# Optimization experiments

Measured on AMD Instinct MI355X. Metric: run time of the kernel, lower is better.

## Reference

```python
import jax, jax.numpy as jnp
import numpy as np

DIMS = [1536, 2048, 2560, 3072, 1792, 2304, 2816, 2048, 2560, 3328]

def _ln(x, g, b, eps=1e-5):
    m = jnp.mean(x, -1, keepdims=True)
    v = jnp.mean((x - m) ** 2, -1, keepdims=True)
    return (x - m) / jnp.sqrt(v + eps) * g + b

def _gelu(x):
    return jax.nn.gelu(x, approximate=False)

def _mish(x):
    return x * jnp.tanh(jax.nn.softplus(x))

_ACTS = [jax.nn.silu, _gelu, _mish, jax.nn.relu, jax.nn.selu, jnp.tanh, jax.nn.softplus, jax.nn.elu]

def _renorm_sparse_topk(probs, active_k, max_k):
    vals, idx = jax.lax.top_k(probs, max_k)
    mask = (jnp.arange(max_k)[None, :] < active_k[:, None]).astype(probs.dtype)
    n = probs.shape[0]
    sparse = jnp.zeros_like(probs).at[jnp.arange(n)[:, None], idx].set(vals * mask)
    return sparse / jnp.clip(jnp.sum(sparse, -1, keepdims=True), 1e-6, None)

def setup_inputs():
    N, IN, OUT, E, M, S, SUB, DST, INNER, SH = 2048, 1024, 10, 10, 24, 4, 4, 40, 768, 2048
    DMAX = max(DIMS)
    ks = iter(jax.random.split(jax.random.key(0), 80))
    def p(shape, std=0.02):
        return jax.random.normal(next(ks), shape, jnp.float32) * std
    eu = np.zeros((E, DMAX, IN), np.float32)
    ed = np.zeros((E, OUT, DMAX), np.float32)
    for i in range(E):
        d = DIMS[i % len(DIMS)]
        eu[i, :d] = np.asarray(p((d, IN), 0.02))
        ed[i, :, :d] = np.asarray(p((OUT, d), 0.01))
    return {
        'x': jax.random.normal(next(ks), (N, IN), jnp.float32),
        'weight': p((OUT, IN), 0.03), 'bias': p((OUT,), 0.01),
        'shared_up_w': p((SH, IN)), 'shared_down_w': p((OUT, SH), 0.01),
        'shared_norm_g': jnp.ones((OUT,)), 'shared_norm_b': jnp.zeros((OUT,)),
        'shared_scale': jnp.asarray(1.0, jnp.float32),
        'memory_keys': p((M, IN)), 'memory_values_init': p((M, IN)),
        'memory_query_w': p((IN, IN), 0.01), 'memory_out_w': p((OUT, IN), 0.01),
        'mem_wgate_w': p((M, 2 * IN), 0.01), 'mem_wgate_b': jnp.zeros((M,)),
        'mem_wval_w': p((IN, IN), 0.01), 'mem_wval_b': jnp.zeros((IN,)),
        'depth_q_w': p((IN, IN), 0.01), 'depth_k_w': p((IN, IN), 0.01),
        'depth_v_w': p((IN, IN), 0.01), 'depth_out_w': p((OUT, IN), 0.01),
        'cell_ln_g': jnp.ones((S, IN)), 'cell_ln_b': jnp.zeros((S, IN)),
        'cell_fc1_w': p((S, INNER, IN)), 'cell_fc1_b': jnp.zeros((S, INNER)),
        'cell_fc2_w': p((S, IN, INNER)), 'cell_fc2_b': jnp.zeros((S, IN)),
        'ssm_a_w': p((DST, IN), 0.01), 'ssm_a_b': jnp.zeros((DST,)),
        'ssm_b_w': p((IN, DST), 0.01), 'ssm_b_b': jnp.zeros((IN,)),
        'mor_sub_w': p((SUB, E, IN)), 'mor_sub_b': jnp.zeros((SUB, E)),
        'mor_mix_w': p((SUB, IN)), 'mor_mix_b': jnp.zeros((SUB,)),
        'expert_bias': jnp.zeros((E,)),
        'budget_w': p((4, IN)), 'budget_b': jnp.zeros((4,)),
        'experts_up': jnp.asarray(eu), 'experts_down': jnp.asarray(ed),
        'expert_norm_g': jnp.ones((E, OUT)), 'expert_norm_b': jnp.zeros((E, OUT)),
        'halt_w': p((S, 1, IN), 0.01), 'halt_b': jnp.full((S, 1), -2.0, jnp.float32),
        'alpha': jnp.asarray(0.1, jnp.float32), 'beta': jnp.asarray(0.1, jnp.float32),
    }

def reference(x, weight, bias, shared_up_w, shared_down_w, shared_norm_g, shared_norm_b, shared_scale, memory_keys, memory_values_init, memory_query_w, memory_out_w, mem_wgate_w, mem_wgate_b, mem_wval_w, mem_wval_b, depth_q_w, depth_k_w, depth_v_w, depth_out_w, cell_ln_g, cell_ln_b, cell_fc1_w, cell_fc1_b, cell_fc2_w, cell_fc2_b, ssm_a_w, ssm_a_b, ssm_b_w, ssm_b_b, mor_sub_w, mor_sub_b, mor_mix_w, mor_mix_b, expert_bias, budget_w, budget_b, experts_up, experts_down, expert_norm_g, expert_norm_b, halt_w, halt_b, alpha, beta):
    in_dim = x.shape[-1]
    x_flat = x.reshape(-1, in_dim)
    n = x_flat.shape[0]
    base = x_flat @ weight.T + bias
    shared = _ln(jax.nn.silu(x_flat @ shared_up_w.T) @ shared_down_w.T, shared_norm_g, shared_norm_b)
    mem_vals = jnp.broadcast_to(memory_values_init[None], (n,) + memory_values_init.shape)
    current = x_flat
    total = jnp.zeros_like(base)
    cum_halt = jnp.zeros((n, 1), x.dtype)
    bank = []
    mem_scale = in_dim ** -0.5
    steps = cell_ln_g.shape[0]
    n_exp = expert_bias.shape[0]
    max_topk = min(4, n_exp)
    for step in range(steps):
        mq = current @ memory_query_w.T
        mem_attn = jax.nn.softmax((mq @ memory_keys.T) * mem_scale, -1)  # [n, M]
        mem_ctx = jnp.einsum('nm,nmd->nd', mem_attn, mem_vals)
        if bank:
            ds = jnp.stack(bank, 1)  # [n, s, d]
            q = current @ depth_q_w.T
            k = ds @ depth_k_w.T
            v = ds @ depth_v_w.T
            attn = jax.nn.softmax(jnp.einsum('nd,nsd->ns', q, k) * mem_scale, -1)
            depth_ctx = jnp.einsum('ns,nsd->nd', attn, v)
        else:
            depth_ctx = jnp.zeros_like(current)
        ssm_corr = jnp.tanh(current @ ssm_a_w.T + ssm_a_b) @ ssm_b_w.T + ssm_b_b
        enriched = current + 0.34 * mem_ctx + 0.22 * depth_ctx + 0.18 * ssm_corr
        h = _gelu(_ln(enriched, cell_ln_g[step], cell_ln_b[step]) @ cell_fc1_w[step].T + cell_fc1_b[step])
        current = enriched + h @ cell_fc2_w[step].T + cell_fc2_b[step]
        bank.append(current)
        sub = jnp.einsum('nd,sed->nse', current, mor_sub_w) + mor_sub_b[None]
        mix = jax.nn.softmax(current @ mor_mix_w.T + mor_mix_b, -1)
        gate_probs = jax.nn.softmax(jnp.einsum('ns,nse->ne', mix, sub) + expert_bias, -1)
        budget = 1 + jnp.argmax(jax.nn.softmax(current @ budget_w.T + budget_b, -1), -1)
        sg = _renorm_sparse_topk(gate_probs, budget, max_topk)
        expert_logits = jnp.zeros_like(base)
        for i in range(n_exp):
            d = DIMS[i % len(DIMS)]
            hh = _ACTS[i % len(_ACTS)](current @ experts_up[i, :d, :].T)
            eo = _ln(hh @ experts_down[i, :, :d].T, expert_norm_g[i], expert_norm_b[i])
            expert_logits = expert_logits + sg[:, i:i + 1] * eo
        step_logits = expert_logits + 0.22 * (mem_ctx @ memory_out_w.T) + 0.14 * (depth_ctx @ depth_out_w.T)
        surprise = 1.0 - jnp.max(sg, -1, keepdims=True)  # [n, 1]
        wg = jax.nn.softmax(jnp.concatenate([current, mem_ctx], -1) @ mem_wgate_w.T + mem_wgate_b, -1)
        wv = (current @ mem_wval_w.T + mem_wval_b)[:, None, :]
        mem_vals = mem_vals + surprise[..., None] * wg[..., None] * (wv - mem_vals)
        halt = jax.nn.sigmoid((current + 0.2 * mem_ctx + 0.1 * depth_ctx) @ halt_w[step].T + halt_b[step])
        remaining = 1.0 - cum_halt
        total = total + remaining * step_logits
        cum_halt = cum_halt + remaining * halt
    total = total / float(steps)
    out = base + shared_scale * shared + (alpha + 1e-4) * total + beta * (current @ memory_out_w.T)
    return out.reshape(x.shape[:-1] + (out.shape[-1],))
```

## Files before the change

### kernel.cpp

```cpp
#include <hip/hip_runtime.h>
#include <stdint.h>

#define N_TOK 2048
#define IN_D  1024
#define NEXP  10
#define NSTEP 4
#define INNER 768
#define SHD   2048
#define DMAX  3328
#define DSUM  24064

typedef __attribute__((ext_vector_type(4))) float f32x4;
typedef __attribute__((ext_vector_type(8))) short bf16x8;

__device__ const int c_dims[10] = {1536,2048,2560,3072,1792,2304,2816,2048,2560,3328};
__device__ const int c_offs[10] = {0,1536,3584,6144,9216,11008,13312,16128,18176,20736};
__device__ const int c_acts[10] = {0,1,2,3,4,5,6,7,0,1};
__device__ const int c_cum[11]  = {0,12,28,48,72,86,104,126,142,162,188};

__device__ __forceinline__ float wred(float v){
#pragma unroll
  for (int s = 32; s > 0; s >>= 1) v += __shfl_xor(v, s, 64);
  return v;
}
// ... 113 lines not shown
}

__global__ void build_routew(const float* __restrict__ msw, const float* __restrict__ mmw,
                             const float* __restrict__ bw, const float* __restrict__ wgw,
                             const float* __restrict__ hw, const float* __restrict__ mow,
                             const float* __restrict__ dow, uint16_t* __restrict__ Wh,
                             uint16_t* __restrict__ Wl){
  const int TOT = 4 * 128 * 3072;
  for (int i = blockIdx.x * 256 + threadIdx.x; i < TOT; i += gridDim.x * 256){
    int t = i / (128 * 3072);
    int rem = i - t * (128 * 3072);
    int row = rem / 3072, col = rem - row * 3072;
    float v = 0.f;
    if (row < 40){ if (col < 1024) v = msw[row * 1024 + col]; }
    else if (row < 44){ if (col < 1024) v = mmw[(row - 40) * 1024 + col]; }
    else if (row < 48){ if (col < 1024) v = bw[(row - 44) * 1024 + col]; }
    else if (row < 72){ if (col < 2048) v = wgw[(row - 48) * 2048 + col]; }
    else if (row == 72){
      if (col < 1024) v = hw[t * 1024 + col];
      else if (col < 2048) v = 0.2f * hw[t * 1024 + col - 1024];
      else v = 0.1f * hw[t * 1024 + col - 2048];
    }
    else if (row < 83){ if (col >= 1024 && col < 2048) v = mow[(row - 73) * 1024 + col - 1024]; }
    else if (row < 93){ if (col >= 2048) v = dow[(row - 83) * 1024 + col - 2048]; }
    else if (row < 103){ if (col < 1024) v = mow[(row - 93) * 1024 + col]; }
    uint16_t h = f2bf(v);
    Wh[i] = h; Wl[i] = f2bf(v - bf2f(h));
  }
}

enum { EPI_GELU=0, EPI_CUR=1, EPI_PRE=2, EPI_QROUTE=3 };

template<int EPI>
__global__ __launch_bounds__(256)
void gemm_sp(const uint16_t* __restrict__ Ah, const uint16_t* __restrict__ Al, int lda,
             const uint16_t* __restrict__ Wh, const uint16_t* __restrict__ Wl,
             const uint16_t* __restrict__ W2h, const uint16_t* __restrict__ W2l,
             const float* __restrict__ bias, const float* __restrict__ addend,
             float* __restrict__ D0, float* __restrict__ D1, float* __restrict__ D2,
             float* __restrict__ D3, uint8_t* __restrict__ o8,
             uint16_t* __restrict__ oH, uint16_t* __restrict__ oL,
             int K, int D)
{
  __shared__ __align__(16) uint16_t sm[4][2][4096];
  int tid = threadIdx.x, lane = tid & 63, wave = tid >> 6;
  int wr = wave >> 1, wc = wave & 1;
  int arow = lane & 15, agrp = lane >> 4;
  int rowBase = blockIdx.y * 128;
  bool isRoute = (EPI == EPI_QROUTE) && ((int)blockIdx.x < 4);
  const uint16_t* Wsh = isRoute ? W2h : Wh;
  const uint16_t* Wsl = isRoute ? W2l : Wl;
  int wst     = isRoute ? 3072 : K;
  int colBase = isRoute ? 0 : ((EPI == EPI_QROUTE ? (int)blockIdx.x - 4 : (int)blockIdx.x) * 128);
  int kBase   = isRoute ? (int)blockIdx.x * 768 : 0;
  int kLen    = isRoute ? 768 : K;
  f32x4 acc[4][4];
#pragma unroll
  for (int m = 0; m < 4; m++)
#pragma unroll
    for (int n = 0; n < 4; n++){ f32x4 z = {0.f,0.f,0.f,0.f}; acc[m][n] = z; }

#define STAGE_G(buf, k0) do { \
  _Pragma("unroll") \
  for (int s = 0; s < 2; s++){ \
    int u = tid + s * 256; \
    int rr = u >> 2; \
    int ch = (u & 3) ^ ((rr >> 1) & 3); \
    size_t ga = (size_t)(rowBase + rr) * lda + kBase + (k0) + ch * 8; \
    size_t gw = (size_t)(colBase + rr) * wst + kBase + (k0) + ch * 8; \
    gload16(&Ah[ga], &sm[0][buf][u << 3]); \
    gload16(&Al[ga], &sm[1][buf][u << 3]); \
    gload16(&Wsh[gw], &sm[2][buf][u << 3]); \
    gload16(&Wsl[gw], &sm[3][buf][u << 3]); \
  } } while(0)

  int nk = kLen >> 5;
  STAGE_G(0, 0);
  if (nk > 1) STAGE_G(1, 32);
  int perm = (arow >> 1) & 3;
#pragma unroll 1
  for (int ki = 0; ki < nk; ki++){
    int cb = ki & 1;
    if (ki + 1 < nk) asm volatile("s_waitcnt vmcnt(8)" ::: "memory");
    else             asm volatile("s_waitcnt vmcnt(0)" ::: "memory");
    __builtin_amdgcn_s_barrier();
    bf16x8 ah[4], al[4], bh[4], bl[4];
#pragma unroll
// ... 19 lines not shown
    __builtin_amdgcn_s_barrier();
    asm volatile("" ::: "memory");
    if (ki + 2 < nk) STAGE_G(cb, (ki + 2) << 5);
  }
#undef STAGE_G
#pragma unroll
  for (int m = 0; m < 4; m++){
#pragma unroll
    for (int n = 0; n < 4; n++){
      int col = colBase + wc*64 + n*16 + arow;
#pragma unroll
      for (int r2 = 0; r2 < 4; r2++){
        int row = rowBase + wr*64 + m*16 + agrp*4 + r2;
        float v = acc[m][n][r2];
        if (EPI == EPI_GELU){
          v += bias[col];
          v = 0.5f * v * (1.f + erff(v * 0.7071067811865475f));
          size_t idx = (size_t)row * D + col;
          uint16_t h = f2bf(v); oH[idx] = h; oL[idx] = f2bf(v - bf2f(h));
        }
        if (EPI == EPI_CUR){
          v += bias[col] + addend[(size_t)row * 1024 + col];
          D0[(size_t)row * 1024 + col] = v;
          size_t idx = (size_t)row * 3072 + col;
          uint16_t h = f2bf(v); oH[idx] = h; oL[idx] = f2bf(v - bf2f(h));
          o8[(size_t)row * 1024 + col] = f2fp8(v);
        }
        if (EPI == EPI_PRE){
          if (col < 2048) D0[(size_t)row * 2048 + col] = v / (1.f + expf(-v));
          else D1[(size_t)row * 128 + col - 2048] = v;
        }
        if (EPI == EPI_QROUTE){
          if (isRoute){
            D3[((size_t)blockIdx.x * N_TOK + row) * 128 + col] = v;
          } else {
            if (col < 1024) D0[(size_t)row * 1024 + col] = v;
            else if (col < 4096) D1[(size_t)row * 3072 + col - 1024] = v + bias[col - 1024];
            else if (col < 4160) D2[(size_t)row * 128 + col - 4096] = v;
          }
        }
      }
    }
  }
}

__global__ __launch_bounds__(256)
void expert_up_mfma(const uint8_t* __restrict__ A8, const uint8_t* __restrict__ U8,
                    const int* __restrict__ cnt, const int* __restrict__ gidx,
                    uint16_t* __restrict__ HH)
{
  int y = blockIdx.y;
  int e = 0;
#pragma unroll
  for (int i = 1; i < 11; i++) if (y >= c_cum[i]) e = i;
  int ct = y - c_cum[e];
  int dcols = c_dims[e];
  int ne = cnt[e];
  const uint8_t* W = U8 + (size_t)e * DMAX * IN_D + (size_t)ct * 128 * IN_D;

  __shared__ __align__(16) uint8_t smem[32768];
  int tid = threadIdx.x, lane = tid & 63, wave = tid >> 6;
  int wr = wave >> 1, wc = wave & 1;
  int arow = lane & 15, agrp = lane >> 4;
  int actid = c_acts[e];
  size_t base_e = (size_t)N_TOK * c_offs[e];
  int rHalf = tid >> 1;
  int half16 = (tid & 1) * 16;

#define STAGE_E(b, k0) do { \
    gload16b(&A8[(size_t)tok * IN_D + (k0) + half16], &smem[(b)*8192 + tid*16]); \
    gload16b(&W[(size_t)rHalf * IN_D + (k0) + half16], &smem[(b)*8192 + 4096 + tid*16]); \
  } while(0)

#pragma unroll 1
  for (int rowBase = blockIdx.x * 128; rowBase < ne; rowBase += 4 * 128){
    int slot = rowBase + rHalf;
    int tok = (slot < ne) ? gidx[e * N_TOK + slot] : 0;

    f32x4 acc[4][4];
#pragma unroll
    for (int m = 0; m < 4; m++)
#pragma unroll
      for (int n = 0; n < 4; n++){ f32x4 z = {0.f,0.f,0.f,0.f}; acc[m][n] = z; }

    STAGE_E(0, 0);
    STAGE_E(1, 32);
    STAGE_E(2, 64);
    int cb = 0;
#pragma unroll 1
    for (int ki = 0; ki < 32; ki++){
      if (ki < 30)       asm volatile("s_waitcnt vmcnt(4)" ::: "memory");
      else if (ki == 30) asm volatile("s_waitcnt vmcnt(2)" ::: "memory");
      else               asm volatile("s_waitcnt vmcnt(0)" ::: "memory");
      __builtin_amdgcn_s_barrier();
      long a[4], b[4];
#pragma unroll
      for (int m = 0; m < 4; m++)
        a[m] = *(const long*)&smem[cb*8192 + (wr*64 + m*16 + arow)*32 + agrp*8];
#pragma unroll
      for (int n = 0; n < 4; n++)
        b[n] = *(const long*)&smem[cb*8192 + 4096 + (wc*64 + n*16 + arow)*32 + agrp*8];
#pragma unroll
      for (int m = 0; m < 4; m++)
#pragma unroll
        for (int n = 0; n < 4; n++)
          acc[m][n] = __builtin_amdgcn_mfma_f32_16x16x32_fp8_fp8(a[m], b[n], acc[m][n], 0, 0, 0);
      __builtin_amdgcn_s_barrier();
      asm volatile("" ::: "memory");
      if (ki + 3 < 32) STAGE_E(cb, (ki + 3) << 5);
      cb = (cb == 2) ? 0 : cb + 1;
    }
    uint16_t* Ht = (uint16_t*)smem;
#pragma unroll
    for (int m = 0; m < 4; m++){
      int rb0 = wr*64 + m*16 + agrp*4;
#pragma unroll
      for (int n = 0; n < 4; n++){
        int col = wc*64 + n*16 + arow;
#pragma unroll
        for (int r2 = 0; r2 < 4; r2++){
          int row = rb0 + r2;
          float v = actf(actid, acc[m][n][r2]);
          Ht[row * 128 + (col ^ ((row & 7) << 3))] = f2bf(v);
        }
      }
    }
    __syncthreads();
#pragma unroll
    for (int i = 0; i < 8; i++){
      int c = tid + i * 256;
      int row = c >> 4, chunk = c & 15;
      int schunk = (chunk & 8) | ((chunk ^ row) & 7);
      int4 val = *(const int4*)&Ht[row * 128 + schunk * 8];
      *(int4*)&HH[base_e + (size_t)(rowBase + row) * dcols
                  + (size_t)ct * 128 + chunk * 8] = val;
    }
    __syncthreads();
  }
#undef STAGE_E
}

__global__ __launch_bounds__(256)
void ctx_enr_kernel(const float* __restrict__ qaux, const float* __restrict__ dqbuf,
                    const float* __restrict__ Ac, const float* __restrict__ W0,
                    const float* __restrict__ W1, const float* __restrict__ W2,
                    const float* __restrict__ mvi,
                    const float* __restrict__ t0, const float* __restrict__ t1,
                    const float* __restrict__ t2, const float* __restrict__ cur,
                    const float* __restrict__ sab, const float* __restrict__ sbw,
                    const float* __restrict__ sbb, const float* __restrict__ lng,
                    const float* __restrict__ lnbv,
                    float* __restrict__ enr, uint16_t* __restrict__ lnh,
                    uint16_t* __restrict__ lnl, uint16_t* __restrict__ Arh,
                    uint16_t* __restrict__ Arl, int t)
{
  int row = blockIdx.x, tid = threadIdx.x;
  __shared__ float su[24], ss[3], s40[40], red[12], redm[8];
  if (tid < 64){
    float pj = (tid < 24) ? qaux[(size_t)row * 128 + tid] * 0.03125f : -1e30f;
    float mx = wmax(pj);
    float ex = (tid < 24) ? expf(pj - mx) : 0.f;
    float sum = wred(ex);
    float attn = ex / sum;
    if (tid < 24) su[tid] = attn * Ac[row * 24 + tid];
    float w0v = (t > 0 && tid < 24) ? W0[row * 24 + tid] : 0.f;
    float s0 = wred(attn * w0v);
    float w1v = (t > 1 && tid < 24) ? W1[row * 24 + tid] : 0.f;
    float s1 = wred(attn * w1v);
    float w2v = (t > 2 && tid < 24) ? W2[row * 24 + tid] : 0.f;
    float s2 = wred(attn * w2v);
    if (tid == 0){ ss[0] = s0; ss[1] = s1; ss[2] = s2; }
    if (tid < 40) s40[tid] = tanhf(qaux[(size_t)row * 128 + 24 + tid] + sab[tid]);
  }
  size_t tb = (size_t)row * 3072;
  if (t > 0){
    float a0 = 0.f, a1 = 0.f, a2 = 0.f;
#pragma unroll
    for (int j = 0; j < 4; j++){
      int d = tid + j * 256;
      float dq = dqbuf[(size_t)row * 1024 + d];
      a0 = fmaf(dq, t0[tb + d], a0);
      if (t > 1) a1 = fmaf(dq, t1[tb + d], a1);
      if (t > 2) a2 = fmaf(dq, t2[tb + d], a2);
    }
    a0 = wred(a0); a1 = wred(a1); a2 = wred(a2);
    if ((tid & 63) == 0){ int w = tid >> 6; red[w] = a0; red[4+w] = a1; red[8+w] = a2; }
  }
  __syncthreads();
  float e0 = 0.f, e1 = 0.f, e2 = 0.f;
// ... 31 lines not shown
#pragma unroll
    for (int o = 0; o < 40; o++) sv = fmaf(s40[o], sbw[d * 40 + o], sv);
    float v = cur[idx] + 0.34f * mv + 0.22f * dv + 0.18f * sv;
    uint16_t mh = f2bf(mv);
    Arh[ar + 1024 + d] = mh; Arl[ar + 1024 + d] = f2bf(mv - bf2f(mh));
    uint16_t dh = f2bf(dv);
    Arh[ar + 2048 + d] = dh; Arl[ar + 2048 + d] = f2bf(dv - bf2f(dh));
    ev[j] = v; part += v;
  }
  part = wred(part);
  if ((tid & 63) == 0) redm[tid >> 6] = part;
  __syncthreads();
  float mean = (redm[0] + redm[1] + redm[2] + redm[3]) * (1.f / 1024.f);
  float vp = 0.f;
#pragma unroll
  for (int j = 0; j < 4; j++){ float dd = ev[j] - mean; vp += dd * dd; }
  vp = wred(vp);
  if ((tid & 63) == 0) redm[4 + (tid >> 6)] = vp;
  __syncthreads();
  float var = (redm[4] + redm[5] + redm[6] + redm[7]) * (1.f / 1024.f);
  float rs = 1.f / sqrtf(var + 1e-5f);
#pragma unroll
  for (int j = 0; j < 4; j++){
    int d = tid + j * 256;
    size_t idx = (size_t)row * IN_D + d;
    enr[idx] = ev[j];
    float v = (ev[j] - mean) * rs * lng[t * IN_D + d] + lnbv[t * IN_D + d];
    uint16_t h = f2bf(v);
    lnh[idx] = h;
    lnl[idx] = f2bf(v - bf2f(h));
  }
}

__global__ __launch_bounds__(256)
void route_fin(const float* __restrict__ ROq, const float* __restrict__ mmb,
               const float* __restrict__ msb, const float* __restrict__ ebias,
               const float* __restrict__ bb, const float* __restrict__ wgb,
               const float* __restrict__ hb,
               float* __restrict__ sg, float* __restrict__ haltb,
               float* __restrict__ Ac, float* __restrict__ W0,
               float* __restrict__ W1, float* __restrict__ W2,
               int* __restrict__ cnt, int* __restrict__ gidx,
               int* __restrict__ pos, float* __restrict__ routeS, int t)
{
  int row = blockIdx.x * 256 + threadIdx.x;
  int lane = threadIdx.x & 63;
  const size_t P = (size_t)N_TOK * 128;
  const float* r0 = ROq + (size_t)row * 128;
  const float* r1 = r0 + P;
  const float* r2 = r0 + 2 * P;
  const float* r3 = r0 + 3 * P;
  auto R = [&](int j){ return r0[j] + r1[j] + r2[j] + r3[j]; };
  float pm[4];
#pragma unroll
  for (int o = 0; o < 4; o++) pm[o] = R(40 + o) + mmb[o];
  float mmx = fmaxf(fmaxf(pm[0], pm[1]), fmaxf(pm[2], pm[3]));
  float msum = 0.f;
#pragma unroll
  for (int o = 0; o < 4; o++){ pm[o] = expf(pm[o] - mmx); msum += pm[o]; }
  float minv = 1.f / msum;
  float gl[10];
#pragma unroll
  for (int e = 0; e < 10; e++){
    float g = ebias[e];
#pragma unroll
    for (int s2 = 0; s2 < 4; s2++)
      g = fmaf(pm[s2] * minv, R(s2 * 10 + e) + msb[s2 * 10 + e], g);
    gl[e] = g;
  }
  float gmx = gl[0];
#pragma unroll
  for (int e = 1; e < 10; e++) gmx = fmaxf(gmx, gl[e]);
  float gs = 0.f;
#pragma unroll
  for (int e = 0; e < 10; e++){ gl[e] = expf(gl[e] - gmx); gs += gl[e]; }
  float ginv = 1.f / gs;
#pragma unroll
  for (int e = 0; e < 10; e++) gl[e] *= ginv;
  float pb0 = R(44) + bb[0], pb1 = R(45) + bb[1], pb2 = R(46) + bb[2], pb3 = R(47) + bb[3];
  int bud = 1; float bbest = pb0;
  if (pb1 > bbest){ bbest = pb1; bud = 2; }
  if (pb2 > bbest){ bbest = pb2; bud = 3; }
  if (pb3 > bbest){ bbest = pb3; bud = 4; }
  float tv[4]; int ti[4]; unsigned used = 0;
#pragma unroll
  for (int j = 0; j < 4; j++){
    float best = -1e30f; int bi = 0;
#pragma unroll
    for (int e = 0; e < 10; e++){
      bool ok = (!((used >> e) & 1u)) && (gl[e] > best);
      if (ok){ best = gl[e]; bi = e; }
    }
    tv[j] = best; ti[j] = bi; used |= (1u << bi);
  }
  float ssum = tv[0];
  if (bud > 1) ssum += tv[1];
  if (bud > 2) ssum += tv[2];
  if (bud > 3) ssum += tv[3];
  float den = fmaxf(ssum, 1e-6f);
  float sup = 1.f - tv[0] / den;
  float sgv[10];
#pragma unroll
  for (int e = 0; e < 10; e++){
    float sv = 0.f;
#pragma unroll
    for (int j = 0; j < 4; j++) if (j < bud && ti[j] == e) sv = tv[j] / den;
    sgv[e] = sv;
    sg[row * 10 + e] = sv;
  }
  float pw[24];
#pragma unroll
  for (int m = 0; m < 24; m++) pw[m] = R(48 + m) + wgb[m];
  float wmx2 = pw[0];
#pragma unroll
  for (int m = 1; m < 24; m++) wmx2 = fmaxf(wmx2, pw[m]);
  float wsum = 0.f;
#pragma unroll
  for (int m = 0; m < 24; m++){ pw[m] = expf(pw[m] - wmx2); wsum += pw[m]; }
  float winv = 1.f / wsum;
#pragma unroll
  for (int m = 0; m < 24; m++){
    float c = sup * pw[m] * winv;
    float om = 1.f - c;
    Ac[row * 24 + m] *= om;
    if (t > 0) W0[row * 24 + m] *= om;
    if (t > 1) W1[row * 24 + m] *= om;
    if (t > 2) W2[row * 24 + m] *= om;
    if (t == 0)      W0[row * 24 + m] = c;
    else if (t == 1) W1[row * 24 + m] = c;
    else if (t == 2) W2[row * 24 + m] = c;
  }
  haltb[row] = 1.f / (1.f + expf(-(R(72) + hb[t])));
#pragma unroll
  for (int i = 0; i < 30; i++) routeS[row * 32 + i] = R(73 + i);
#pragma unroll
  for (int e = 0; e < 10; e++){
    bool act = sgv[e] != 0.f;
    unsigned long long mask = __ballot(act);
    int cw = __popcll(mask);
    int b0 = 0;
    if (lane == 0 && cw > 0) b0 = atomicAdd(&cnt[e], cw);
    b0 = __shfl(b0, 0, 64);
    if (act){
      int slot = b0 + __popcll(mask & ((1ull << lane) - 1ull));
      gidx[e * N_TOK + slot] = row;
      pos[row * 10 + e] = slot;
    }
  }
}

__global__ __launch_bounds__(256)
void downfin_kernel(const uint16_t* __restrict__ HH, const int* __restrict__ pos,
                    const float* __restrict__ ED, const float* __restrict__ sg,
                    const float* __restrict__ eng, const float* __restrict__ enb,
                    const float* __restrict__ routeS, const float* __restrict__ haltb,
                    float* __restrict__ total, float* __restrict__ cumh)
{
  int lane = threadIdx.x & 63;
  int row = blockIdx.x * 4 + (threadIdx.x >> 6);
  float out[10] = {};
  for (int e = 0; e < NEXP; e++){
    float g = sg[row * 10 + e];
    if (g != 0.0f){
      int d = c_dims[e];
      int slot = pos[row * 10 + e];
      const uint16_t* hr = HH + (size_t)N_TOK * c_offs[e] + (size_t)slot * d;
      const float* wd = ED + (size_t)e * 10 * DMAX;
      float p[10] = {};
      for (int k = lane * 4; k < d; k += 256){
        uint2 hv = *(const uint2*)&hr[k];
        float h0 = bf2f((uint16_t)hv.x), h1 = bf2f((uint16_t)(hv.x >> 16));
        float h2 = bf2f((uint16_t)hv.y), h3 = bf2f((uint16_t)(hv.y >> 16));
#pragma unroll
        for (int o = 0; o < 10; o++){
          float4 w4 = *(const float4*)&wd[o * DMAX + k];
          p[o] = fmaf(h0, w4.x, fmaf(h1, w4.y, fmaf(h2, w4.z, fmaf(h3, w4.w, p[o]))));
        }
      }
#pragma unroll
      for (int o = 0; o < 10; o++) p[o] = wred(p[o]);
      float mean = 0.f;
#pragma unroll
      for (int o = 0; o < 10; o++) mean += p[o];
      mean *= 0.1f;
      float var = 0.f;
#pragma unroll
      for (int o = 0; o < 10; o++){ float dd = p[o] - mean; var += dd * dd; }
      var *= 0.1f;
      float rs = 1.f / sqrtf(var + 1e-5f);
#pragma unroll
      for (int o = 0; o < 10; o++)
        out[o] += g * ((p[o] - mean) * rs * eng[e * 10 + o] + enb[e * 10 + o]);
    }
  }
  if (lane == 0){
    const float* r = routeS + (size_t)row * 32;
    float rem = 1.f - cumh[row];
#pragma unroll
    for (int o = 0; o < 10; o++)
      total[row * 10 + o] += rem * (out[o] + 0.22f * r[o] + 0.14f * r[10 + o]);
    cumh[row] += rem * haltb[row];
  }
}

__global__ __launch_bounds__(256)
void shared_kernel(const float* __restrict__ shpre, const float* __restrict__ sdw,
                   const float* __restrict__ g, const float* __restrict__ b,
                   float* __restrict__ outp)
{
  int lane = threadIdx.x & 63;
  int row = blockIdx.x * 4 + (threadIdx.x >> 6);
  const float* xr = shpre + (size_t)row * SHD;
  float p[10];
#pragma unroll
  for (int o = 0; o < 10; o++) p[o] = 0.f;
  for (int k = lane; k < SHD; k += 64){
    float xv = xr[k];
#pragma unroll
    for (int o = 0; o < 10; o++) p[o] = fmaf(xv, sdw[o * SHD + k], p[o]);
  }
#pragma unroll
  for (int o = 0; o < 10; o++) p[o] = wred(p[o]);
  float mean = 0.f;
#pragma unroll
  for (int o = 0; o < 10; o++) mean += p[o];
  mean *= 0.1f;
  float var = 0.f;
#pragma unroll
  for (int o = 0; o < 10; o++){ float dd = p[o] - mean; var += dd * dd; }
  var *= 0.1f;
  float rs = 1.f / sqrtf(var + 1e-5f);
  if (lane == 0){
#pragma unroll
    for (int o = 0; o < 10; o++) outp[row * 10 + o] = (p[o] - mean) * rs * g[o] + b[o];
// ... 125 lines not shown
  hipMemsetAsync(cbias, 0, 3072 * 4, stream);
  hipMemcpyAsync(cbias + 2048, wvb, 1024 * 4, hipMemcpyDeviceToDevice, stream);
  hipMemcpyAsync(cur, x, NI * 4, hipMemcpyDeviceToDevice, stream);
  fill1_kernel<<<(N_TOK * 24 + 255) / 256, 256, 0, stream>>>(Ac, N_TOK * 24);
  cvt_fp8_kernel<<<2048, 256, 0, stream>>>(eup, upbf8, (size_t)NEXP * DMAX * IN_D);

  split_strided<<<1024, 256, 0, stream>>>(x, Arh, Arl, N_TOK, 1024, 3072);
  split_kernel<<<1024, 256, 0, stream>>>(suw, preWh, preWl, (size_t)SHD * 1024);
  split_kernel<<<256, 256, 0, stream>>>(saw, preWh + (size_t)2072*1024, preWl + (size_t)2072*1024, (size_t)40 * 1024);
  split_kernel<<<256, 256, 0, stream>>>(wgt, preWh + (size_t)2112*1024, preWl + (size_t)2112*1024, (size_t)10 * 1024);
  hipMemsetAsync(preWh + (size_t)2122*1024, 0, (size_t)54 * 1024 * 2, stream);
  hipMemsetAsync(preWl + (size_t)2122*1024, 0, (size_t)54 * 1024 * 2, stream);
  split_kernel<<<1024, 256, 0, stream>>>(dqw, qtWh, qtWl, W1M);
  split_kernel<<<1024, 256, 0, stream>>>(dkw, qtWh + W1M, qtWl + W1M, W1M);
  split_kernel<<<1024, 256, 0, stream>>>(dvw, qtWh + 2*W1M, qtWl + 2*W1M, W1M);
  split_kernel<<<1024, 256, 0, stream>>>(wvw, qtWh + 3*W1M, qtWl + 3*W1M, W1M);
  split_kernel<<<256, 256, 0, stream>>>(saw, qtWh + (size_t)4120*1024, qtWl + (size_t)4120*1024, (size_t)40 * 1024);
  hipMemsetAsync(qtWh + (size_t)4160*1024, 0, (size_t)64 * 1024 * 2, stream);
  hipMemsetAsync(qtWl + (size_t)4160*1024, 0, (size_t)64 * 1024 * 2, stream);
  k2_kernel<<<dim3(24, 4), 256, 0, stream>>>(keys, mqw, K2f);
  split_kernel<<<256, 256, 0, stream>>>(K2f, preWh + (size_t)2048*1024, preWl + (size_t)2048*1024, (size_t)24 * 1024);
  split_kernel<<<256, 256, 0, stream>>>(K2f, qtWh + (size_t)4096*1024, qtWl + (size_t)4096*1024, (size_t)24 * 1024);
  build_routew<<<2048, 256, 0, stream>>>(msw, mmw, bw, wgw, hw, mow, dow, rtWh, rtWl);
  split_kernel<<<1024, 256, 0, stream>>>(fc1w, fc1wh, fc1wl, WFC);
  split_kernel<<<1024, 256, 0, stream>>>(fc2w, fc2wh, fc2wl, WFC);

  gemm_sp<EPI_PRE><<<dim3(17, 16), 256, 0, stream>>>(
      Arh, Arl, 3072, preWh, preWl, nullptr, nullptr, nullptr, nullptr,
      shpre, qaux, nullptr, nullptr, nullptr, nullptr, nullptr, IN_D, 2176);
  shared_kernel<<<512, 256, 0, stream>>>(shpre, sdw, sng, snb, sharedp);

  float* trioB[3] = {trio0, trio1, trio2};

  for (int t = 0; t < NSTEP; t++){
    ctx_enr_kernel<<<2048, 256, 0, stream>>>(qaux, dqbuf, Ac, W0, W1, W2, mvi,
                                             trio0, trio1, trio2, cur, sab, sbw, sbb,
                                             clng, clnb, enr, lnh, lnl, Arh, Arl, t);
    gemm_sp<EPI_GELU><<<dim3(INNER/128, 16), 256, 0, stream>>>(
        lnh, lnl, 1024, fc1wh + (size_t)t * INNER * IN_D, fc1wl + (size_t)t * INNER * IN_D,
        nullptr, nullptr, fc1b + t * INNER, nullptr,
        nullptr, nullptr, nullptr, nullptr, nullptr, h7h, h7l, IN_D, INNER);
    gemm_sp<EPI_CUR><<<dim3(8, 16), 256, 0, stream>>>(
        h7h, h7l, 768, fc2wh + (size_t)t * IN_D * INNER, fc2wl + (size_t)t * IN_D * INNER,
        nullptr, nullptr, fc2b + t * IN_D, enr,
        cur, nullptr, nullptr, nullptr, A8, Arh, Arl, INNER, IN_D);
    gemm_sp<EPI_QROUTE><<<dim3(t < 3 ? 37 : 4, 16), 256, 0, stream>>>(
        Arh, Arl, 3072, qtWh, qtWl,
        rtWh + (size_t)t * 128 * 3072, rtWl + (size_t)t * 128 * 3072,
        cbias, nullptr, dqbuf, t < 3 ? trioB[t] : nullptr, qaux, routeQ,
        nullptr, nullptr, nullptr, IN_D, 4224);
    route_fin<<<8, 256, 0, stream>>>(routeQ, mmb, msb, ebias, bb, wgb, hb,
                                     sg, haltb, Ac, W0, W1, W2,
                                     cnt + t * 16, gidx, pos, routeS, t);
    expert_up_mfma<<<dim3(4, 188), 256, 0, stream>>>(A8, upbf8, cnt + t * 16, gidx, HHc);
    downfin_kernel<<<512, 256, 0, stream>>>(HHc, pos, edn, sg, eng, enb,
                                            routeS, haltb, total, cumh);
  }
  final_lite<<<8, 256, 0, stream>>>(qaux, bias, sharedp, total, routeS,
                                    sscale, alphap, betap, outp);
}
```

Before: 2.202 ms.

## Co-schedule independent kernels via horizontal fusion and swizzle expert LDS layout

The per-step ctx kernel for step t+1 now runs in the same launch as the expert-up GEMM of step t, and the expert-down/finalize work of step t-1 shares a launch with the fc1 GEMM of step t. Block-index ranges select which core runs, so fewer launches are needed and under-filled grids can overlap on the GPU. The expert-up kernel also swizzles its LDS staging and read offsets to cut bank conflicts. This relies on the fused parts having no data dependency on each other. The bigger blocks may also lower occupancy.

```diff
diff --git a/kernel.cpp b/kernel.cpp
--- a/kernel.cpp
+++ b/kernel.cpp
@@ -169,27 +169,27 @@
 enum { EPI_GELU=0, EPI_CUR=1, EPI_PRE=2, EPI_QROUTE=3 };
 
 template<int EPI>
-__global__ __launch_bounds__(256)
-void gemm_sp(const uint16_t* __restrict__ Ah, const uint16_t* __restrict__ Al, int lda,
-             const uint16_t* __restrict__ Wh, const uint16_t* __restrict__ Wl,
-             const uint16_t* __restrict__ W2h, const uint16_t* __restrict__ W2l,
-             const float* __restrict__ bias, const float* __restrict__ addend,
-             float* __restrict__ D0, float* __restrict__ D1, float* __restrict__ D2,
-             float* __restrict__ D3, uint8_t* __restrict__ o8,
-             uint16_t* __restrict__ oH, uint16_t* __restrict__ oL,
-             int K, int D)
-{
-  __shared__ __align__(16) uint16_t sm[4][2][4096];
+__device__ __forceinline__
+void gemm_core(uint16_t (*sm)[2][4096], int bx, int by,
+               const uint16_t* __restrict__ Ah, const uint16_t* __restrict__ Al, int lda,
+               const uint16_t* __restrict__ Wh, const uint16_t* __restrict__ Wl,
+               const uint16_t* __restrict__ W2h, const uint16_t* __restrict__ W2l,
+               const float* __restrict__ bias, const float* __restrict__ addend,
+               float* __restrict__ D0, float* __restrict__ D1, float* __restrict__ D2,
+               float* __restrict__ D3, uint8_t* __restrict__ o8,
+               uint16_t* __restrict__ oH, uint16_t* __restrict__ oL,
+               int K, int D)
+{
   int tid = threadIdx.x, lane = tid & 63, wave = tid >> 6;
   int wr = wave >> 1, wc = wave & 1;
   int arow = lane & 15, agrp = lane >> 4;
-  int rowBase = blockIdx.y * 128;
-  bool isRoute = (EPI == EPI_QROUTE) && ((int)blockIdx.x < 4);
+  int rowBase = by * 128;
+  bool isRoute = (EPI == EPI_QROUTE) && (bx < 4);
   const uint16_t* Wsh = isRoute ? W2h : Wh;
   const uint16_t* Wsl = isRoute ? W2l : Wl;
   int wst     = isRoute ? 3072 : K;
-  int colBase = isRoute ? 0 : ((EPI == EPI_QROUTE ? (int)blockIdx.x - 4 : (int)blockIdx.x) * 128);
-  int kBase   = isRoute ? (int)blockIdx.x * 768 : 0;
+  int colBase = isRoute ? 0 : ((EPI == EPI_QROUTE ? bx - 4 : bx) * 128);
+  int kBase   = isRoute ? bx * 768 : 0;
   int kLen    = isRoute ? 768 : K;
   f32x4 acc[4][4];
 #pragma unroll
@@ -275,7 +275,7 @@
         }
         if (EPI == EPI_QROUTE){
           if (isRoute){
-            D3[((size_t)blockIdx.x * N_TOK + row) * 128 + col] = v;
+            D3[((size_t)bx * N_TOK + row) * 128 + col] = v;
           } else {
             if (col < 1024) D0[(size_t)row * 1024 + col] = v;
             else if (col < 4096) D1[(size_t)row * 3072 + col - 1024] = v + bias[col - 1024];
@@ -287,36 +287,36 @@
   }
 }
 
-__global__ __launch_bounds__(256)
-void expert_up_mfma(const uint8_t* __restrict__ A8, const uint8_t* __restrict__ U8,
-                    const int* __restrict__ cnt, const int* __restrict__ gidx,
-                    uint16_t* __restrict__ HH)
-{
-  int y = blockIdx.y;
+__device__ __forceinline__
+void expert_core(uint8_t* smem, int ex, int ey,
+                 const uint8_t* __restrict__ A8, const uint8_t* __restrict__ U8,
+                 const int* __restrict__ cnt, const int* __restrict__ gidx,
+                 uint16_t* __restrict__ HH)
+{
   int e = 0;
 #pragma unroll
-  for (int i = 1; i < 11; i++) if (y >= c_cum[i]) e = i;
-  int ct = y - c_cum[e];
+  for (int i = 1; i < 11; i++) if (ey >= c_cum[i]) e = i;
+  int ct = ey - c_cum[e];
   int dcols = c_dims[e];
   int ne = cnt[e];
   const uint8_t* W = U8 + (size_t)e * DMAX * IN_D + (size_t)ct * 128 * IN_D;
 
-  __shared__ __align__(16) uint8_t smem[32768];
   int tid = threadIdx.x, lane = tid & 63, wave = tid >> 6;
   int wr = wave >> 1, wc = wave & 1;
   int arow = lane & 15, agrp = lane >> 4;
   int actid = c_acts[e];
   size_t base_e = (size_t)N_TOK * c_offs[e];
   int rHalf = tid >> 1;
-  int half16 = (tid & 1) * 16;
+  int h16 = (((tid & 1) ^ ((tid >> 3) & 1)) << 4);
+  int off = ((((agrp >> 1) ^ ((arow >> 2) & 1)) << 4) | ((agrp & 1) << 3));
 
 #define STAGE_E(b, k0) do { \
-    gload16b(&A8[(size_t)tok * IN_D + (k0) + half16], &smem[(b)*8192 + tid*16]); \
-    gload16b(&W[(size_t)rHalf * IN_D + (k0) + half16], &smem[(b)*8192 + 4096 + tid*16]); \
+    gload16b(&A8[(size_t)tok * IN_D + (k0) + h16], &smem[(b)*8192 + tid*16]); \
+    gload16b(&W[(size_t)rHalf * IN_D + (k0) + h16], &smem[(b)*8192 + 4096 + tid*16]); \
   } while(0)
 
 #pragma unroll 1
-  for (int rowBase = blockIdx.x * 128; rowBase < ne; rowBase += 4 * 128){
+  for (int rowBase = ex * 128; rowBase < ne; rowBase += 4 * 128){
     int slot = rowBase + rHalf;
     int tok = (slot < ne) ? gidx[e * N_TOK + slot] : 0;
 
@@ -339,10 +339,10 @@
       long a[4], b[4];
 #pragma unroll
       for (int m = 0; m < 4; m++)
-        a[m] = *(const long*)&smem[cb*8192 + (wr*64 + m*16 + arow)*32 + agrp*8];
+        a[m] = *(const long*)&smem[cb*8192 + (wr*64 + m*16 + arow)*32 + off];
 #pragma unroll
       for (int n = 0; n < 4; n++)
-        b[n] = *(const long*)&smem[cb*8192 + 4096 + (wc*64 + n*16 + arow)*32 + agrp*8];
+        b[n] = *(const long*)&smem[cb*8192 + 4096 + (wc*64 + n*16 + arow)*32 + off];
 #pragma unroll
       for (int m = 0; m < 4; m++)
 #pragma unroll
@@ -383,21 +383,22 @@
 #undef STAGE_E
 }
 
-__global__ __launch_bounds__(256)
-void ctx_enr_kernel(const float* __restrict__ qaux, const float* __restrict__ dqbuf,
-                    const float* __restrict__ Ac, const float* __restrict__ W0,
-                    const float* __restrict__ W1, const float* __restrict__ W2,
-                    const float* __restrict__ mvi,
-                    const float* __restrict__ t0, const float* __restrict__ t1,
-                    const float* __restrict__ t2, const float* __restrict__ cur,
-                    const float* __restrict__ sab, const float* __restrict__ sbw,
-                    const float* __restrict__ sbb, const float* __restrict__ lng,
-                    const float* __restrict__ lnbv,
-                    float* __restrict__ enr, uint16_t* __restrict__ lnh,
-                    uint16_t* __restrict__ lnl, uint16_t* __restrict__ Arh,
-                    uint16_t* __restrict__ Arl, int t)
-{
-  int row = blockIdx.x, tid = threadIdx.x;
+__device__ __forceinline__
+void ctx_core(int row, int t,
+              const float* __restrict__ qaux, const float* __restrict__ dqbuf,
+              const float* __restrict__ Ac, const float* __restrict__ W0,
+              const float* __restrict__ W1, const float* __restrict__ W2,
+              const float* __restrict__ mvi,
+              const float* __restrict__ t0, const float* __restrict__ t1,
+              const float* __restrict__ t2, const float* __restrict__ cur,
+              const float* __restrict__ sab, const float* __restrict__ sbw,
+              const float* __restrict__ sbb, const float* __restrict__ lng,
+              const float* __restrict__ lnbv,
+              float* __restrict__ enr, uint16_t* __restrict__ lnh,
+              uint16_t* __restrict__ lnl, uint16_t* __restrict__ Arh,
+              uint16_t* __restrict__ Arl)
+{
+  int tid = threadIdx.x;
   __shared__ float su[24], ss[3], s40[40], red[12], redm[8];
   if (tid < 64){
     float pj = (tid < 24) ? qaux[(size_t)row * 128 + tid] * 0.03125f : -1e30f;
@@ -495,132 +496,16 @@
   }
 }
 
-__global__ __launch_bounds__(256)
-void route_fin(const float* __restrict__ ROq, const float* __restrict__ mmb,
-               const float* __restrict__ msb, const float* __restrict__ ebias,
-               const float* __restrict__ bb, const float* __restrict__ wgb,
-               const float* __restrict__ hb,
-               float* __restrict__ sg, float* __restrict__ haltb,
-               float* __restrict__ Ac, float* __restrict__ W0,
-               float* __restrict__ W1, float* __restrict__ W2,
-               int* __restrict__ cnt, int* __restrict__ gidx,
-               int* __restrict__ pos, float* __restrict__ routeS, int t)
-{
-  int row = blockIdx.x * 256 + threadIdx.x;
+__device__ __forceinline__
+void down_core(int rowblk,
+               const uint16_t* __restrict__ HH, const int* __restrict__ pos,
+               const float* __restrict__ ED, const float* __restrict__ sg,
+               const float* __restrict__ eng, const float* __restrict__ enb,
+               const float* __restrict__ routeS, const float* __restrict__ haltb,
+               float* __restrict__ total, float* __restrict__ cumh)
+{
   int lane = threadIdx.x & 63;
-  const size_t P = (size_t)N_TOK * 128;
-  const float* r0 = ROq + (size_t)row * 128;
-  const float* r1 = r0 + P;
-  const float* r2 = r0 + 2 * P;
-  const float* r3 = r0 + 3 * P;
-  auto R = [&](int j){ return r0[j] + r1[j] + r2[j] + r3[j]; };
-  float pm[4];
-#pragma unroll
-  for (int o = 0; o < 4; o++) pm[o] = R(40 + o) + mmb[o];
-  float mmx = fmaxf(fmaxf(pm[0], pm[1]), fmaxf(pm[2], pm[3]));
-  float msum = 0.f;
-#pragma unroll
-  for (int o = 0; o < 4; o++){ pm[o] = expf(pm[o] - mmx); msum += pm[o]; }
-  float minv = 1.f / msum;
-  float gl[10];
-#pragma unroll
-  for (int e = 0; e < 10; e++){
-    float g = ebias[e];
-#pragma unroll
-    for (int s2 = 0; s2 < 4; s2++)
-      g = fmaf(pm[s2] * minv, R(s2 * 10 + e) + msb[s2 * 10 + e], g);
-    gl[e] = g;
-  }
-  float gmx = gl[0];
-#pragma unroll
-  for (int e = 1; e < 10; e++) gmx = fmaxf(gmx, gl[e]);
-  float gs = 0.f;
-#pragma unroll
-  for (int e = 0; e < 10; e++){ gl[e] = expf(gl[e] - gmx); gs += gl[e]; }
-  float ginv = 1.f / gs;
-#pragma unroll
-  for (int e = 0; e < 10; e++) gl[e] *= ginv;
-  float pb0 = R(44) + bb[0], pb1 = R(45) + bb[1], pb2 = R(46) + bb[2], pb3 = R(47) + bb[3];
-  int bud = 1; float bbest = pb0;
-  if (pb1 > bbest){ bbest = pb1; bud = 2; }
-  if (pb2 > bbest){ bbest = pb2; bud = 3; }
-  if (pb3 > bbest){ bbest = pb3; bud = 4; }
-  float tv[4]; int ti[4]; unsigned used = 0;
-#pragma unroll
-  for (int j = 0; j < 4; j++){
-    float best = -1e30f; int bi = 0;
-#pragma unroll
-    for (int e = 0; e < 10; e++){
-      bool ok = (!((used >> e) & 1u)) && (gl[e] > best);
-      if (ok){ best = gl[e]; bi = e; }
-    }
-    tv[j] = best; ti[j] = bi; used |= (1u << bi);
-  }
-  float ssum = tv[0];
-  if (bud > 1) ssum += tv[1];
-  if (bud > 2) ssum += tv[2];
-  if (bud > 3) ssum += tv[3];
-  float den = fmaxf(ssum, 1e-6f);
-  float sup = 1.f - tv[0] / den;
-  float sgv[10];
-#pragma unroll
-  for (int e = 0; e < 10; e++){
-    float sv = 0.f;
-#pragma unroll
-    for (int j = 0; j < 4; j++) if (j < bud && ti[j] == e) sv = tv[j] / den;
-    sgv[e] = sv;
-    sg[row * 10 + e] = sv;
-  }
-  float pw[24];
-#pragma unroll
-  for (int m = 0; m < 24; m++) pw[m] = R(48 + m) + wgb[m];
-  float wmx2 = pw[0];
-#pragma unroll
-  for (int m = 1; m < 24; m++) wmx2 = fmaxf(wmx2, pw[m]);
-  float wsum = 0.f;
-#pragma unroll
-  for (int m = 0; m < 24; m++){ pw[m] = expf(pw[m] - wmx2); wsum += pw[m]; }
-  float winv = 1.f / wsum;
-#pragma unroll
-  for (int m = 0; m < 24; m++){
-    float c = sup * pw[m] * winv;
-    float om = 1.f - c;
-    Ac[row * 24 + m] *= om;
-    if (t > 0) W0[row * 24 + m] *= om;
-    if (t > 1) W1[row * 24 + m] *= om;
-    if (t > 2) W2[row * 24 + m] *= om;
-    if (t == 0)      W0[row * 24 + m] = c;
-    else if (t == 1) W1[row * 24 + m] = c;
-    else if (t == 2) W2[row * 24 + m] = c;
-  }
-  haltb[row] = 1.f / (1.f + expf(-(R(72) + hb[t])));
-#pragma unroll
-  for (int i = 0; i < 30; i++) routeS[row * 32 + i] = R(73 + i);
-#pragma unroll
-  for (int e = 0; e < 10; e++){
-    bool act = sgv[e] != 0.f;
-    unsigned long long mask = __ballot(act);
-    int cw = __popcll(mask);
-    int b0 = 0;
-    if (lane == 0 && cw > 0) b0 = atomicAdd(&cnt[e], cw);
-    b0 = __shfl(b0, 0, 64);
-    if (act){
-      int slot = b0 + __popcll(mask & ((1ull << lane) - 1ull));
-      gidx[e * N_TOK + slot] = row;
-      pos[row * 10 + e] = slot;
-    }
-  }
-}
-
-__global__ __launch_bounds__(256)
-void downfin_kernel(const uint16_t* __restrict__ HH, const int* __restrict__ pos,
-                    const float* __restrict__ ED, const float* __restrict__ sg,
-                    const float* __restrict__ eng, const float* __restrict__ enb,
-                    const float* __restrict__ routeS, const float* __restrict__ haltb,
-                    float* __restrict__ total, float* __restrict__ cumh)
-{
-  int lane = threadIdx.x & 63;
-  int row = blockIdx.x * 4 + (threadIdx.x >> 6);
+  int row = rowblk * 4 + (threadIdx.x >> 6);
   float out[10] = {};
   for (int e = 0; e < NEXP; e++){
     float g = sg[row * 10 + e];
@@ -663,6 +548,216 @@
     for (int o = 0; o < 10; o++)
       total[row * 10 + o] += rem * (out[o] + 0.22f * r[o] + 0.14f * r[10 + o]);
     cumh[row] += rem * haltb[row];
+  }
+}
+
+template<int EPI>
+__global__ __launch_bounds__(256)
+void gemm_sp(const uint16_t* __restrict__ Ah, const uint16_t* __restrict__ Al, int lda,
+             const uint16_t* __restrict__ Wh, const uint16_t* __restrict__ Wl,
+             const uint16_t* __restrict__ W2h, const uint16_t* __restrict__ W2l,
+             const float* __restrict__ bias, const float* __restrict__ addend,
+             float* __restrict__ D0, float* __restrict__ D1, float* __restrict__ D2,
+             float* __restrict__ D3, uint8_t* __restrict__ o8,
+             uint16_t* __restrict__ oH, uint16_t* __restrict__ oL,
+             int K, int D)
+{
+  __shared__ __align__(16) uint16_t sm[4][2][4096];
+  gemm_core<EPI>(sm, blockIdx.x, blockIdx.y, Ah, Al, lda, Wh, Wl, W2h, W2l,
+                 bias, addend, D0, D1, D2, D3, o8, oH, oL, K, D);
+}
+
+__global__ __launch_bounds__(256)
+void fused_fc1_down(const uint16_t* __restrict__ lnh, const uint16_t* __restrict__ lnl,
+                    const uint16_t* __restrict__ fc1h, const uint16_t* __restrict__ fc1l,
+                    const float* __restrict__ fc1b,
+                    uint16_t* __restrict__ h7h, uint16_t* __restrict__ h7l,
+                    const uint16_t* __restrict__ HH, const int* __restrict__ pos,
+                    const float* __restrict__ ED, const float* __restrict__ sg,
+                    const float* __restrict__ eng, const float* __restrict__ enb,
+                    const float* __restrict__ routeS, const float* __restrict__ haltb,
+                    float* __restrict__ total, float* __restrict__ cumh)
+{
+  __shared__ __align__(16) uint16_t sm[4][2][4096];
+  int bid = blockIdx.x;
+  if (bid < 96){
+    gemm_core<EPI_GELU>(sm, bid % 6, bid / 6, lnh, lnl, 1024, fc1h, fc1l,
+                        nullptr, nullptr, fc1b, nullptr,
+                        nullptr, nullptr, nullptr, nullptr, nullptr,
+                        h7h, h7l, IN_D, INNER);
+  } else {
+    down_core(bid - 96, HH, pos, ED, sg, eng, enb, routeS, haltb, total, cumh);
+  }
+}
+
+__global__ __launch_bounds__(256)
+void fused_exp_ctx(const uint8_t* __restrict__ A8, const uint8_t* __restrict__ U8,
+                   const int* __restrict__ cnt, const int* __restrict__ gidx,
+                   uint16_t* __restrict__ HH,
+                   const float* __restrict__ qaux, const float* __restrict__ dqbuf,
+                   const float* __restrict__ Ac, const float* __restrict__ W0,
+                   const float* __restrict__ W1, const float* __restrict__ W2,
+                   const float* __restrict__ mvi,
+                   const float* __restrict__ t0, const float* __restrict__ t1,
+                   const float* __restrict__ t2, const float* __restrict__ cur,
+                   const float* __restrict__ sab, const float* __restrict__ sbw,
+                   const float* __restrict__ sbb, const float* __restrict__ lng,
+                   const float* __restrict__ lnbv,
+                   float* __restrict__ enr, uint16_t* __restrict__ lnh,
+                   uint16_t* __restrict__ lnl, uint16_t* __restrict__ Arh,
+                   uint16_t* __restrict__ Arl, int tn)
+{
+  __shared__ __align__(16) uint8_t smem[32768];
+  int bid = blockIdx.x;
+  if (bid < 752){
+    expert_core(smem, bid & 3, bid >> 2, A8, U8, cnt, gidx, HH);
+  } else {
+    ctx_core(bid - 752, tn, qaux, dqbuf, Ac, W0, W1, W2, mvi, t0, t1, t2,
+             cur, sab, sbw, sbb, lng, lnbv, enr, lnh, lnl, Arh, Arl);
+  }
+}
+
+__global__ __launch_bounds__(256)
+void ctx_kernel(const float* __restrict__ qaux, const float* __restrict__ dqbuf,
+                const float* __restrict__ Ac, const float* __restrict__ W0,
+                const float* __restrict__ W1, const float* __restrict__ W2,
+                const float* __restrict__ mvi,
+                const float* __restrict__ t0, const float* __restrict__ t1,
+                const float* __restrict__ t2, const float* __restrict__ cur,
+                const float* __restrict__ sab, const float* __restrict__ sbw,
+                const float* __restrict__ sbb, const float* __restrict__ lng,
+                const float* __restrict__ lnbv,
+                float* __restrict__ enr, uint16_t* __restrict__ lnh,
+                uint16_t* __restrict__ lnl, uint16_t* __restrict__ Arh,
+                uint16_t* __restrict__ Arl, int t)
+{
+  ctx_core(blockIdx.x, t, qaux, dqbuf, Ac, W0, W1, W2, mvi, t0, t1, t2,
+           cur, sab, sbw, sbb, lng, lnbv, enr, lnh, lnl, Arh, Arl);
+}
+__global__ __launch_bounds__(256)
+void down_kernel(const uint16_t* __restrict__ HH, const int* __restrict__ pos,
+                 const float* __restrict__ ED, const float* __restrict__ sg,
+                 const float* __restrict__ eng, const float* __restrict__ enb,
+                 const float* __restrict__ routeS, const float* __restrict__ haltb,
+                 float* __restrict__ total, float* __restrict__ cumh)
+{
+  down_core(blockIdx.x, HH, pos, ED, sg, eng, enb, routeS, haltb, total, cumh);
+}
+
+__global__ __launch_bounds__(256)
+void route_fin(const float* __restrict__ ROq, const float* __restrict__ mmb,
+               const float* __restrict__ msb, const float* __restrict__ ebias,
+               const float* __restrict__ bb, const float* __restrict__ wgb,
+               const float* __restrict__ hb,
+               float* __restrict__ sg, float* __restrict__ haltb,
+               float* __restrict__ Ac, float* __restrict__ W0,
+               float* __restrict__ W1, float* __restrict__ W2,
+               int* __restrict__ cnt, int* __restrict__ gidx,
+               int* __restrict__ pos, float* __restrict__ routeS, int t)
+{
+  int row = blockIdx.x * 256 + threadIdx.x;
+  int lane = threadIdx.x & 63;
+  const size_t P = (size_t)N_TOK * 128;
+  const float* r0 = ROq + (size_t)row * 128;
+  const float* r1 = r0 + P;
+  const float* r2 = r0 + 2 * P;
+  const float* r3 = r0 + 3 * P;
+  auto R = [&](int j){ return r0[j] + r1[j] + r2[j] + r3[j]; };
+  float pm[4];
+#pragma unroll
+  for (int o = 0; o < 4; o++) pm[o] = R(40 + o) + mmb[o];
+  float mmx = fmaxf(fmaxf(pm[0], pm[1]), fmaxf(pm[2], pm[3]));
+  float msum = 0.f;
+#pragma unroll
+  for (int o = 0; o < 4; o++){ pm[o] = expf(pm[o] - mmx); msum += pm[o]; }
+  float minv = 1.f / msum;
+  float gl[10];
+#pragma unroll
+  for (int e = 0; e < 10; e++){
+    float g = ebias[e];
+#pragma unroll
+    for (int s2 = 0; s2 < 4; s2++)
+      g = fmaf(pm[s2] * minv, R(s2 * 10 + e) + msb[s2 * 10 + e], g);
+    gl[e] = g;
+  }
+  float gmx = gl[0];
+#pragma unroll
+  for (int e = 1; e < 10; e++) gmx = fmaxf(gmx, gl[e]);
+  float gs = 0.f;
+#pragma unroll
+  for (int e = 0; e < 10; e++){ gl[e] = expf(gl[e] - gmx); gs += gl[e]; }
+  float ginv = 1.f / gs;
+#pragma unroll
+  for (int e = 0; e < 10; e++) gl[e] *= ginv;
+  float pb0 = R(44) + bb[0], pb1 = R(45) + bb[1], pb2 = R(46) + bb[2], pb3 = R(47) + bb[3];
+  int bud = 1; float bbest = pb0;
+  if (pb1 > bbest){ bbest = pb1; bud = 2; }
+  if (pb2 > bbest){ bbest = pb2; bud = 3; }
+  if (pb3 > bbest){ bbest = pb3; bud = 4; }
+  float tv[4]; int ti[4]; unsigned used = 0;
+#pragma unroll
+  for (int j = 0; j < 4; j++){
+    float best = -1e30f; int bi = 0;
+#pragma unroll
+    for (int e = 0; e < 10; e++){
+      bool ok = (!((used >> e) & 1u)) && (gl[e] > best);
+      if (ok){ best = gl[e]; bi = e; }
+    }
+    tv[j] = best; ti[j] = bi; used |= (1u << bi);
+  }
+  float ssum = tv[0];
+  if (bud > 1) ssum += tv[1];
+  if (bud > 2) ssum += tv[2];
+  if (bud > 3) ssum += tv[3];
+  float den = fmaxf(ssum, 1e-6f);
+  float sup = 1.f - tv[0] / den;
+  float sgv[10];
+#pragma unroll
+  for (int e = 0; e < 10; e++){
+    float sv = 0.f;
+#pragma unroll
+    for (int j = 0; j < 4; j++) if (j < bud && ti[j] == e) sv = tv[j] / den;
+    sgv[e] = sv;
+    sg[row * 10 + e] = sv;
+  }
+  float pw[24];
+#pragma unroll
+  for (int m = 0; m < 24; m++) pw[m] = R(48 + m) + wgb[m];
+  float wmx2 = pw[0];
+#pragma unroll
+  for (int m = 1; m < 24; m++) wmx2 = fmaxf(wmx2, pw[m]);
+  float wsum = 0.f;
+#pragma unroll
+  for (int m = 0; m < 24; m++){ pw[m] = expf(pw[m] - wmx2); wsum += pw[m]; }
+  float winv = 1.f / wsum;
+#pragma unroll
+  for (int m = 0; m < 24; m++){
+    float c = sup * pw[m] * winv;
+    float om = 1.f - c;
+    Ac[row * 24 + m] *= om;
+    if (t > 0) W0[row * 24 + m] *= om;
+    if (t > 1) W1[row * 24 + m] *= om;
+    if (t > 2) W2[row * 24 + m] *= om;
+    if (t == 0)      W0[row * 24 + m] = c;
+    else if (t == 1) W1[row * 24 + m] = c;
+    else if (t == 2) W2[row * 24 + m] = c;
+  }
+  haltb[row] = 1.f / (1.f + expf(-(R(72) + hb[t])));
+#pragma unroll
+  for (int i = 0; i < 30; i++) routeS[row * 32 + i] = R(73 + i);
+#pragma unroll
+  for (int e = 0; e < 10; e++){
+    bool act = sgv[e] != 0.f;
+    unsigned long long mask = __ballot(act);
+    int cw = __popcll(mask);
+    int b0 = 0;
+    if (lane == 0 && cw > 0) b0 = atomicAdd(&cnt[e], cw);
+    b0 = __shfl(b0, 0, 64);
+    if (act){
+      int slot = b0 + __popcll(mask & ((1ull << lane) - 1ull));
+      gidx[e * N_TOK + slot] = row;
+      pos[row * 10 + e] = slot;
+    }
   }
 }
 
@@ -854,14 +949,15 @@
 
   float* trioB[3] = {trio0, trio1, trio2};
 
+  ctx_kernel<<<2048, 256, 0, stream>>>(qaux, dqbuf, Ac, W0, W1, W2, mvi,
+                                       trio0, trio1, trio2, cur, sab, sbw, sbb,
+                                       clng, clnb, enr, lnh, lnl, Arh, Arl, 0);
+
   for (int t = 0; t < NSTEP; t++){
-    ctx_enr_kernel<<<2048, 256, 0, stream>>>(qaux, dqbuf, Ac, W0, W1, W2, mvi,
-                                             trio0, trio1, trio2, cur, sab, sbw, sbb,
-                                             clng, clnb, enr, lnh, lnl, Arh, Arl, t);
-    gemm_sp<EPI_GELU><<<dim3(INNER/128, 16), 256, 0, stream>>>(
-        lnh, lnl, 1024, fc1wh + (size_t)t * INNER * IN_D, fc1wl + (size_t)t * INNER * IN_D,
-        nullptr, nullptr, fc1b + t * INNER, nullptr,
-        nullptr, nullptr, nullptr, nullptr, nullptr, h7h, h7l, IN_D, INNER);
+    fused_fc1_down<<<(t > 0 ? 608 : 96), 256, 0, stream>>>(
+        lnh, lnl, fc1wh + (size_t)t * INNER * IN_D, fc1wl + (size_t)t * INNER * IN_D,
+        fc1b + t * INNER, h7h, h7l,
+        HHc, pos, edn, sg, eng, enb, routeS, haltb, total, cumh);
     gemm_sp<EPI_CUR><<<dim3(8, 16), 256, 0, stream>>>(
         h7h, h7l, 768, fc2wh + (size_t)t * IN_D * INNER, fc2wl + (size_t)t * IN_D * INNER,
         nullptr, nullptr, fc2b + t * IN_D, enr,
@@ -874,10 +970,13 @@
     route_fin<<<8, 256, 0, stream>>>(routeQ, mmb, msb, ebias, bb, wgb, hb,
                                      sg, haltb, Ac, W0, W1, W2,
                                      cnt + t * 16, gidx, pos, routeS, t);
-    expert_up_mfma<<<dim3(4, 188), 256, 0, stream>>>(A8, upbf8, cnt + t * 16, gidx, HHc);
-    downfin_kernel<<<512, 256, 0, stream>>>(HHc, pos, edn, sg, eng, enb,
-                                            routeS, haltb, total, cumh);
-  }
+    fused_exp_ctx<<<(t < 3 ? 2800 : 752), 256, 0, stream>>>(
+        A8, upbf8, cnt + t * 16, gidx, HHc,
+        qaux, dqbuf, Ac, W0, W1, W2, mvi, trio0, trio1, trio2, cur,
+        sab, sbw, sbb, clng, clnb, enr, lnh, lnl, Arh, Arl, t + 1);
+  }
+  down_kernel<<<512, 256, 0, stream>>>(HHc, pos, edn, sg, eng, enb,
+                                       routeS, haltb, total, cumh);
   final_lite<<<8, 256, 0, stream>>>(qaux, bias, sharedp, total, routeS,
                                     sscale, alphap, betap, outp);
 }
```

Result: slower. 2.322 ms (+5.5%).
